# Kernel tuning notes

Measured on AMD Instinct MI355X. Metric: run time of the kernel, lower is better.

## Reference

```python
import jax, jax.numpy as jnp
import numpy as np

ENT_TOTAL = 100000
REL_TOTAL = 1000
HIDDEN = 128
BATCH_SEQ = 8192  # 2 * batch_size (pos + neg halves)
MARGIN = 1.0
LAMB = 0.01
REG = 0.01


def setup_inputs() -> dict:
    key = jax.random.key(0)
    k0, k1, k2 = jax.random.split(key, 3)
    # [batch_seq, 3] index triples (h, r, t); values valid for both tables
    inp = jax.random.randint(k0, (BATCH_SEQ, 3), 0, REL_TOTAL, dtype=jnp.int64)
    # xavier-ish embedding tables
    scale = 1.0 / np.sqrt(HIDDEN)
    ent_emb = jax.random.normal(k1, (ENT_TOTAL, HIDDEN), dtype=jnp.float32) * scale
    rel_emb = jax.random.normal(k2, (REL_TOTAL, HIDDEN), dtype=jnp.float32) * scale
    Wr = jnp.zeros((REL_TOTAL, HIDDEN, HIDDEN), dtype=jnp.float32)
    return {"input": inp, "ent_emb": ent_emb, "rel_emb": rel_emb, "Wr": Wr}


def reference(input, ent_emb, rel_emb, Wr):
    bs = input.shape[0] // 2
    # gather embeddings (torch code keeps a singleton middle dim; we squeeze it)
    h = ent_emb[input[:, 0]]  # [2bs, H]
    r = rel_emb[input[:, 1]]
    t = ent_emb[input[:, 2]]
    error = jnp.abs(h + r - t)  # [2bs, H]
    ep, en = error[:bs], error[bs:]

    # relWr[b] = en_b en_b^T - ep_b ep_b^T  (abs-error outer products)
    relWr = jnp.einsum('bh,bk->bhk', en, en) - jnp.einsum('bh,bk->bhk', ep, ep)

    # matching torch scatter_ nondeterministic overwrite semantics)
    pos_r = input[:bs, 1]
    Wr_new = Wr.at[pos_r].set(relWr)

    # quadratic-form cross scores: p[i, j] = ep_i^T relWr_j ep_j (torch broadcast matmul semantics)
    vp = jnp.einsum('jhk,jk->jh', relWr, ep)  # [bs, H]
    vn = jnp.einsum('jhk,jk->jh', relWr, en)
    p_score = ep @ vp.T  # [bs, bs]
    n_score = en @ vn.T

    margin_loss = jnp.sum(jax.nn.relu(p_score - n_score + MARGIN)) / bs
    wr_loss = jnp.linalg.norm(relWr.reshape(-1)) * LAMB  # Frobenius (p=2) norm
    norm_loss = (jnp.linalg.norm(h.reshape(-1)) + jnp.linalg.norm(r.reshape(-1))
                 + jnp.linalg.norm(t.reshape(-1))) * REG
    loss = margin_loss + wr_loss + norm_loss
    return (loss, Wr_new)
```

## Files before the change

### kernel.cpp

```cpp
#include <hip/hip_runtime.h>
#include <hip/hip_bf16.h>
#include <math.h>

#define HID 128
#define BSEQ 8192
#define BSH 4096
#define RELS 1000
#define KEXT 256
#define NTILE 64
#define NTRI 2080

typedef unsigned int u32;
typedef unsigned short u16;
typedef __attribute__((ext_vector_type(8))) short bf16x8;
typedef __attribute__((ext_vector_type(4))) float f32x4;


__device__ inline u16 f2bf(float x) {
    u32 u = __float_as_uint(x);
    u32 r = (u + 0x7fff + ((u >> 16) & 1)) >> 16;
    return (u16)r;
}

__device__ inline u32 pack2bf(float x) {
    u16 hi = f2bf(x);
    float hf = __uint_as_float((u32)hi << 16);
    u16 lo = f2bf(x - hf);
    return (u32)hi | ((u32)lo << 16);
}

#define GLOAD_LDS16(g, l) __builtin_amdgcn_global_load_lds( \
    (const __attribute__((address_space(1))) u32*)(g), \
    (__attribute__((address_space(3))) u32*)(l), 16, 0, 0)

__global__ void k_init(int* __restrict__ winner) {
    int t = blockIdx.x * blockDim.x + threadIdx.x;
    if (t < RELS) winner[t] = -1;
}

__global__ __launch_bounds__(256) void k_prep(const int* __restrict__ idx,
                                              const float* __restrict__ ent,
                                              const float* __restrict__ rel,
                                              float* __restrict__ e,
                                              u32* __restrict__ S,
                                              float* __restrict__ abc,
                                              int* __restrict__ winner,
                                              double* __restrict__ part) {
    const int b = blockIdx.x;
    const int half = threadIdx.x >> 7;
    const int k = threadIdx.x & 127;
    const int row = half ? (b + BSH) : b;
    const int i0 = idx[row * 3 + 0];
    const int i1 = idx[row * 3 + 1];
    const int i2 = idx[row * 3 + 2];
    const float h = ent[(size_t)i0 * HID + k];
    const float r = rel[(size_t)i1 * HID + k];
    const float t = ent[(size_t)i2 * HID + k];
    const float val = fabsf(h + r - t);
    e[(size_t)row * HID + k] = val;

    __shared__ float sE[2][128];
    __shared__ float sh[3][4];
    __shared__ float sPart[3][2];
    sE[half][k] = val;

    float hh = h * h, rr = r * r, tt = t * t;
    #pragma unroll
    for (int off = 32; off; off >>= 1) {
        hh += __shfl_down(hh, off);
        rr += __shfl_down(rr, off);
        tt += __shfl_down(tt, off);
    }
    int lane = threadIdx.x & 63, wv = threadIdx.x >> 6;
    if (lane == 0) { sh[0][wv] = hh; sh[1][wv] = rr; sh[2][wv] = tt; }
    __syncthreads();

    const float p = sE[0][k], n = sE[1][k];
    {
        size_t base = ((size_t)(1 + half) * BSH + b) * (KEXT / 2);
        S[base + k] = pack2bf(val);
        if (half == 0) {
            size_t ub = (size_t)b * (KEXT / 2);
            S[ub + k] = pack2bf(p + n);
        }
    }
    if (half == 0) {
        float ak = p * n, bk = p * p, ck = n * n;
        #pragma unroll
        for (int off = 32; off; off >>= 1) {
            ak += __shfl_down(ak, off);
            bk += __shfl_down(bk, off);
            ck += __shfl_down(ck, off);
        }
        if (lane == 0) { sPart[0][wv] = ak; sPart[1][wv] = bk; sPart[2][wv] = ck; }
    }
    __syncthreads();
    if (threadIdx.x == 0) {
        float a = sPart[0][0] + sPart[0][1];
        float bb = sPart[1][0] + sPart[1][1];
        float c = sPart[2][0] + sPart[2][1];
        abc[b] = a; abc[BSH + b] = bb; abc[2 * BSH + b] = c;
        double ad = a, bd = bb, cd = c;
        part[(size_t)b * 4 + 0] = (double)(sh[0][0] + sh[0][1] + sh[0][2] + sh[0][3]);
        part[(size_t)b * 4 + 1] = (double)(sh[1][0] + sh[1][1] + sh[1][2] + sh[1][3]);
        part[(size_t)b * 4 + 2] = (double)(sh[2][0] + sh[2][1] + sh[2][2] + sh[2][3]);
        part[(size_t)b * 4 + 3] = cd * cd - 2.0 * ad * ad + bd * bd;
        atomicMax(&winner[i1], b);
    }
}

__device__ __forceinline__ void stage_chunk(const u16* __restrict__ S,
                                            int I0, int J0, int wv, int lane,
                                            int kc, u16* lds) {
    #pragma unroll
    for (int qq = 0; qq < 6; ++qq) {
        int q = wv * 6 + qq;
        int b = q * 1024 + lane * 16;
        int arr = b >> 12;
        int within = b & 4095;
        int row = within >> 6;
        int colB = within & 63;
        int m = arr >> 1;
        int R0 = (arr & 1) ? J0 : I0;
        int sbl = (colB >> 4) ^ ((row >> 1) & 3);
        const u16* src = S + ((size_t)(m * BSH + R0 + row) << 8)
                           + kc * 32 + (sbl << 3);
        GLOAD_LDS16(src, &lds[q * 512]);
    }
}

__global__ __launch_bounds__(256) void k_scoremm(const u16* __restrict__ S,
                                                 const float* __restrict__ abc,
                                                 double* __restrict__ pm) {
    const int f = blockIdx.x;
    int bi = (int)(64.5f - sqrtf(64.5f * 64.5f - 2.0f * (float)f));
    while ((bi + 1) * NTILE - ((bi + 1) * bi) / 2 <= f) ++bi;
    while (bi * NTILE - (bi * (bi - 1)) / 2 > f) --bi;
    const int bj = bi + (f - (bi * NTILE - (bi * (bi - 1)) / 2));
    const int I0 = bi * 64, J0 = bj * 64;

    __shared__ __align__(16) u16 sAll[2][6 * 64 * 32];
    __shared__ float sRed[4];
    const int t = threadIdx.x;
    const int lane = t & 63, wv = t >> 6;
    const int wr = wv >> 1, wc = wv & 1;
    const int lam = lane & 15, lag = lane >> 4;
    const int swz = (lam >> 1) & 3;
    const int fofs = ((lag ^ swz) << 3);

    f32x4 a0[2][2] = {}, a1[2][2] = {}, a2[2][2] = {};

    stage_chunk(S, I0, J0, wv, lane, 0, sAll[0]);
    stage_chunk(S, I0, J0, wv, lane, 1, sAll[1]);

#define KSTEP(KC, NWAIT)                                                      \
    {                                                                         \
        asm volatile("s_waitcnt vmcnt(" #NWAIT ")" ::: "memory");             \
        __builtin_amdgcn_sched_barrier(0);                                    \
        __builtin_amdgcn_s_barrier();                                         \
        __builtin_amdgcn_sched_barrier(0);                                    \
        const u16* buf = sAll[KC & 1];                                        \
        bf16x8 fa[3][2], fb[3][2];                                            \
        _Pragma("unroll")                                                     \
        for (int m = 0; m < 3; ++m) {                                         \
            _Pragma("unroll")                                                 \
            for (int ff = 0; ff < 2; ++ff) {                                  \
                fa[m][ff] = *(const bf16x8*)&buf[(m * 2 + 0) * 2048           \
                               + (wr * 32 + ff * 16 + lam) * 32 + fofs];      \
                fb[m][ff] = *(const bf16x8*)&buf[(m * 2 + 1) * 2048           \
                               + (wc * 32 + ff * 16 + lam) * 32 + fofs];      \
            }                                                                 \
        }                                                                     \
        asm volatile("s_waitcnt lgkmcnt(0)" ::: "memory");                    \
        __builtin_amdgcn_sched_barrier(0);                                    \
        __builtin_amdgcn_s_barrier();                                         \
        __builtin_amdgcn_sched_barrier(0);                                    \
        if ((KC) + 2 < 8)                                                     \
            stage_chunk(S, I0, J0, wv, lane, (KC) + 2, sAll[KC & 1]);         \
        _Pragma("unroll")                                                     \
        for (int fi = 0; fi < 2; ++fi) {                                      \
            _Pragma("unroll")                                                 \
            for (int fj = 0; fj < 2; ++fj) {                                  \
                a0[fi][fj] = __builtin_amdgcn_mfma_f32_16x16x32_bf16(         \
                    fa[0][fi], fb[0][fj], a0[fi][fj], 0, 0, 0);               \
                a1[fi][fj] = __builtin_amdgcn_mfma_f32_16x16x32_bf16(         \
                    fa[1][fi], fb[1][fj], a1[fi][fj], 0, 0, 0);               \
                a2[fi][fj] = __builtin_amdgcn_mfma_f32_16x16x32_bf16(         \
                    fa[2][fi], fb[2][fj], a2[fi][fj], 0, 0, 0);               \
            }                                                                 \
        }                                                                     \
    }

    KSTEP(0, 6) KSTEP(1, 6) KSTEP(2, 6) KSTEP(3, 6)
    KSTEP(4, 6) KSTEP(5, 6) KSTEP(6, 6) KSTEP(7, 0)
#undef KSTEP

    const float* A = abc;
    const float* Bv = abc + BSH;
    const float* Cv = abc + 2 * BSH;
    float lsum = 0.f;
    #pragma unroll
    for (int fj = 0; fj < 2; ++fj) {
        int j = J0 + wc * 32 + fj * 16 + lam;
        float aj = A[j], abj = aj + Bv[j], acj = aj + Cv[j];
        #pragma unroll
        for (int fi = 0; fi < 2; ++fi)
            #pragma unroll
            for (int r = 0; r < 4; ++r) {
                float s = fmaf(aj, a0[fi][fj][r], 1.0f)
                          - abj * a1[fi][fj][r] - acj * a2[fi][fj][r];
                lsum += fmaxf(s, 0.f);
            }
    }
    if (bj != bi) {
        #pragma unroll
        for (int fi = 0; fi < 2; ++fi)
            #pragma unroll
            for (int r = 0; r < 4; ++r) {
                int i = I0 + wr * 32 + fi * 16 + lag * 4 + r;
                float ai = A[i], abi = ai + Bv[i], aci = ai + Cv[i];
                #pragma unroll
                for (int fj = 0; fj < 2; ++fj) {
                    float s = fmaf(ai, a0[fi][fj][r], 1.0f)
                              - abi * a1[fi][fj][r] - aci * a2[fi][fj][r];
                    lsum += fmaxf(s, 0.f);
                }
            }
    }
    #pragma unroll
    for (int off = 32; off; off >>= 1) lsum += __shfl_down(lsum, off);
    if (lane == 0) sRed[wv] = lsum;
    __syncthreads();
    if (t == 0)
        pm[f] = (double)(sRed[0] + sRed[1] + sRed[2] + sRed[3]);
}

__global__ __launch_bounds__(256) void k_reduce(const double* __restrict__ pp,
                                                const double* __restrict__ pm,
                                                float* __restrict__ out) {
    int t = threadIdx.x;
    double h2 = 0, r2 = 0, t2 = 0, wr = 0, mg = 0;
    for (int i = t; i < BSH; i += 256) {
        h2 += pp[(size_t)i * 4 + 0];
        r2 += pp[(size_t)i * 4 + 1];
        t2 += pp[(size_t)i * 4 + 2];
        wr += pp[(size_t)i * 4 + 3];
        if (i < NTRI) mg += pm[i];
    }
    #pragma unroll
    for (int off = 32; off; off >>= 1) {
        h2 += __shfl_down(h2, off);
        r2 += __shfl_down(r2, off);
        t2 += __shfl_down(t2, off);
        wr += __shfl_down(wr, off);
        mg += __shfl_down(mg, off);
    }
    __shared__ double sred[5][4];
    int lane = t & 63, wv = t >> 6;
    if (lane == 0) {
        sred[0][wv] = h2; sred[1][wv] = r2; sred[2][wv] = t2;
        sred[3][wv] = wr; sred[4][wv] = mg;
    }
    __syncthreads();
    if (t == 0) {
        double H = sred[0][0] + sred[0][1] + sred[0][2] + sred[0][3];
        double R = sred[1][0] + sred[1][1] + sred[1][2] + sred[1][3];
        double T = sred[2][0] + sred[2][1] + sred[2][2] + sred[2][3];
        double W = sred[3][0] + sred[3][1] + sred[3][2] + sred[3][3];
        double M = sred[4][0] + sred[4][1] + sred[4][2] + sred[4][3];
        out[0] = (float)(M / (double)BSH + sqrt(W) * 0.01
                         + (sqrt(H) + sqrt(R) + sqrt(T)) * 0.01);
    }
}

__global__ __launch_bounds__(256) void k_wrout(const float* __restrict__ Wr,
                                               const float* __restrict__ e,
                                               const int* __restrict__ winner,
                                               float* __restrict__ outWr) {
    int rel = blockIdx.x;
    int t = threadIdx.x;
    float* out = outWr + (size_t)rel * HID * HID;
    int j = winner[rel];
    if (j < 0) {
        const float* src = Wr + (size_t)rel * HID * HID;
        #pragma unroll 8
        for (int it = 0; it < 64; ++it) out[it * 256 + t] = src[it * 256 + t];
    } else {
        __shared__ float sep[HID], sen[HID];
        if (t < 128) sep[t] = e[(size_t)j * HID + t];
        else sen[t - 128] = e[(size_t)(j + BSH) * HID + (t - 128)];
        __syncthreads();
        #pragma unroll 8
        for (int it = 0; it < 64; ++it) {
            int ix = it * 256 + t;
            int hh = ix >> 7, kk = ix & 127;
            out[ix] = sen[hh] * sen[kk] - sep[hh] * sep[kk];
        }
    }
}

extern "C" void kernel_launch(void* const* d_in, const int* in_sizes, int n_in,
                              void* d_out, int out_size, void* d_ws, size_t ws_size,
                              hipStream_t stream) {
    const int* idx = (const int*)d_in[0];
    const float* ent = (const float*)d_in[1];
    const float* rel = (const float*)d_in[2];
    const float* Wr = (const float*)d_in[3];
    float* out = (float*)d_out;

    char* ws = (char*)d_ws;
    int* winner = (int*)(ws + 64);
    float* abc = (float*)(ws + 4096);
    float* e = (float*)(ws + 53248);
    u32* S = (u32*)(out + 4);
    double* pp = (double*)((char*)d_out + 6291488);
    double* pm = (double*)((char*)d_out + 6422560);

    k_init<<<4, 256, 0, stream>>>(winner);
    k_prep<<<BSH, 256, 0, stream>>>(idx, ent, rel, e, S, abc, winner, pp);
    k_scoremm<<<NTRI, 256, 0, stream>>>((const u16*)S, abc, pm);
    k_reduce<<<1, 256, 0, stream>>>(pp, pm, out);
    k_wrout<<<RELS, 256, 0, stream>>>(Wr, e, winner, out + 1);
}
```

Before: 211.4 us.

## Triple-buffer score-GEMM LDS staging, drop second barrier, remap tile order

Grows the LDS staging ring for the triangular score-matrix GEMM from two to three buffers. The prefetch of chunk k+2 is now issued before the current chunk's LDS reads, so the second workgroup barrier per k-step can go. Fragment loads become hand-written ds_read_b128 with immediate offsets instead of compiler-generated address arithmetic. Block IDs are also interleaved across the triangle to spread work and memory traffic. In exchange, LDS use per block rises, which may lower occupancy, and the inline asm loads bypass compiler scheduling and must stay consistent with the vmcnt waits.

```diff
diff --git a/kernel.cpp b/kernel.cpp
--- a/kernel.cpp
+++ b/kernel.cpp
@@ -32,6 +32,10 @@
 #define GLOAD_LDS16(g, l) __builtin_amdgcn_global_load_lds( \
     (const __attribute__((address_space(1))) u32*)(g), \
     (__attribute__((address_space(3))) u32*)(l), 16, 0, 0)
+
+#define DSR(dst, addrv, OFF) \
+    asm volatile("ds_read_b128 %0, %1 offset:" #OFF \
+                 : "=v"(dst) : "v"(addrv))
 
 __global__ void k_init(int* __restrict__ winner) {
     int t = blockIdx.x * blockDim.x + threadIdx.x;
@@ -132,26 +136,34 @@
 __global__ __launch_bounds__(256) void k_scoremm(const u16* __restrict__ S,
                                                  const float* __restrict__ abc,
                                                  double* __restrict__ pm) {
-    const int f = blockIdx.x;
+    const int bid = blockIdx.x;
+    const int f = (bid & 7) * (NTRI / 8) + (bid >> 3);
     int bi = (int)(64.5f - sqrtf(64.5f * 64.5f - 2.0f * (float)f));
     while ((bi + 1) * NTILE - ((bi + 1) * bi) / 2 <= f) ++bi;
     while (bi * NTILE - (bi * (bi - 1)) / 2 > f) --bi;
     const int bj = bi + (f - (bi * NTILE - (bi * (bi - 1)) / 2));
     const int I0 = bi * 64, J0 = bj * 64;
 
-    __shared__ __align__(16) u16 sAll[2][6 * 64 * 32];
+    __shared__ __align__(16) u16 sAll[3][6 * 64 * 32];
     __shared__ float sRed[4];
     const int t = threadIdx.x;
     const int lane = t & 63, wv = t >> 6;
     const int wr = wv >> 1, wc = wv & 1;
     const int lam = lane & 15, lag = lane >> 4;
     const int swz = (lam >> 1) & 3;
-    const int fofs = ((lag ^ swz) << 3);
+    const unsigned fof = (unsigned)((lag ^ swz) << 4);
+
+    const unsigned lbase =
+        (unsigned)(unsigned long long)(__attribute__((address_space(3))) u16*)
+            (u16*)&sAll[0][0];
+    const unsigned aA0 = lbase + wr * 2048 + lam * 64 + fof;
+    const unsigned aB0 = lbase + 4096 + wc * 2048 + lam * 64 + fof;
 
     f32x4 a0[2][2] = {}, a1[2][2] = {}, a2[2][2] = {};
-
-    stage_chunk(S, I0, J0, wv, lane, 0, sAll[0]);
-    stage_chunk(S, I0, J0, wv, lane, 1, sAll[1]);
+    bf16x8 fa[3][2], fb[3][2];
+
+    stage_chunk(S, I0, J0, wv, lane, 0, &sAll[0][0]);
+    stage_chunk(S, I0, J0, wv, lane, 1, &sAll[1][0]);
 
 #define KSTEP(KC, NWAIT)                                                      \
     {                                                                         \
@@ -159,24 +171,19 @@
         __builtin_amdgcn_sched_barrier(0);                                    \
         __builtin_amdgcn_s_barrier();                                         \
         __builtin_amdgcn_sched_barrier(0);                                    \
-        const u16* buf = sAll[KC & 1];                                        \
-        bf16x8 fa[3][2], fb[3][2];                                            \
-        _Pragma("unroll")                                                     \
-        for (int m = 0; m < 3; ++m) {                                         \
-            _Pragma("unroll")                                                 \
-            for (int ff = 0; ff < 2; ++ff) {                                  \
-                fa[m][ff] = *(const bf16x8*)&buf[(m * 2 + 0) * 2048           \
-                               + (wr * 32 + ff * 16 + lam) * 32 + fofs];      \
-                fb[m][ff] = *(const bf16x8*)&buf[(m * 2 + 1) * 2048           \
-                               + (wc * 32 + ff * 16 + lam) * 32 + fofs];      \
-            }                                                                 \
-        }                                                                     \
+        if ((KC) + 2 < 8)                                                     \
+            stage_chunk(S, I0, J0, wv, lane, (KC) + 2,                        \
+                        &sAll[((KC) + 2) % 3][0]);                            \
+        const unsigned aA = aA0 + ((KC) % 3) * 24576u;                        \
+        const unsigned aB = aB0 + ((KC) % 3) * 24576u;                        \
+        DSR(fa[0][0], aA, 0);     DSR(fa[0][1], aA, 1024);                    \
+        DSR(fa[1][0], aA, 8192);  DSR(fa[1][1], aA, 9216);                    \
+        DSR(fa[2][0], aA, 16384); DSR(fa[2][1], aA, 17408);                   \
+        DSR(fb[0][0], aB, 0);     DSR(fb[0][1], aB, 1024);                    \
+        DSR(fb[1][0], aB, 8192);  DSR(fb[1][1], aB, 9216);                    \
+        DSR(fb[2][0], aB, 16384); DSR(fb[2][1], aB, 17408);                   \
         asm volatile("s_waitcnt lgkmcnt(0)" ::: "memory");                    \
         __builtin_amdgcn_sched_barrier(0);                                    \
-        __builtin_amdgcn_s_barrier();                                         \
-        __builtin_amdgcn_sched_barrier(0);                                    \
-        if ((KC) + 2 < 8)                                                     \
-            stage_chunk(S, I0, J0, wv, lane, (KC) + 2, sAll[KC & 1]);         \
         _Pragma("unroll")                                                     \
         for (int fi = 0; fi < 2; ++fi) {                                      \
             _Pragma("unroll")                                                 \
```

New measurement: 215.4 us. No clear change (+1.9%).
